# Kernel optimization log

Hardware: AMD Instinct MI355X
Metric: run time of the kernel (lower is better)

The kernel has to match this reference:

```python
import jax, jax.numpy as jnp
import numpy as np
import math

B, N, DEG, C, F0, NCLS = 128, 512, 8, 128, 128, 10
E = B * N * DEG
RATIO = 0.8
K1 = math.ceil(RATIO * N)    # 410
K2 = math.ceil(RATIO * K1)   # 328
K3 = math.ceil(RATIO * K2)   # 263


def setup_inputs() -> dict:
    key = jax.random.key(0)
    ks = jax.random.split(key, 32)
    x = jax.random.normal(ks[0], (B * N, F0), jnp.float32)
    epg = N * DEG
    src_l = jax.random.randint(ks[1], (B, epg), 0, N)
    dst_l = jax.random.randint(ks[2], (B, epg), 0, N)
    off = (jnp.arange(B, dtype=jnp.int32) * N)[:, None]
    edge_src = (src_l + off).reshape(-1).astype(jnp.int32)
    edge_dst = (dst_l + off).reshape(-1).astype(jnp.int32)

    def lin(k, fi, fo):
        return jax.random.normal(k, (fi, fo), jnp.float32) / np.float32(np.sqrt(fi))

    inp = {"x": x, "edge_src": edge_src, "edge_dst": edge_dst}
    i = 3
    for s, fi in (("1", F0), ("2", C), ("3", C)):
        inp["Wroot" + s] = lin(ks[i], fi, C); i += 1
        inp["Wrel" + s] = lin(ks[i], fi, C); i += 1
        inp["brel" + s] = jnp.zeros((C,), jnp.float32)
        inp["p" + s] = jax.random.normal(ks[i], (C,), jnp.float32); i += 1
    inp["W1"] = lin(ks[i], 2 * C, 128); i += 1
    inp["b1"] = jnp.zeros((128,), jnp.float32)
    inp["W2"] = lin(ks[i], 128, 64); i += 1
    inp["b2"] = jnp.zeros((64,), jnp.float32)
    inp["W3"] = lin(ks[i], 64, NCLS); i += 1
    inp["b3"] = jnp.zeros((NCLS,), jnp.float32)
    return inp


def graph_conv(x, src, dst, emask, Wroot, Wrel, brel, num_nodes):
    # PyG GraphConv (aggr='add'): lin_rel(sum_j x_j) + lin_root(x_i)
    msg = x[src] * emask[:, None]                      # masked gather  [E, C]
    agg = jax.ops.segment_sum(msg, dst, num_segments=num_nodes)
    return agg @ Wrel + brel + x @ Wroot


def topk_pool(x, p, src, dst, emask, b, n, k):
    # score = tanh(x . p / ||p||), keep top-k nodes per graph, scale kept x by score
    score = jnp.tanh((x @ p) / jnp.linalg.norm(p))     # [b*n]
    vals, idx = jax.lax.top_k(score.reshape(b, n), k)  # [b, k]
    perm = (idx + (jnp.arange(b, dtype=idx.dtype) * n)[:, None]).reshape(-1)
    x_new = x[perm] * vals.reshape(-1, 1)
    inv = jnp.full((b * n,), -1, jnp.int32).at[perm].set(
        jnp.arange(b * k, dtype=jnp.int32))
    ns, nd = inv[src], inv[dst]
    nmask = emask * (ns >= 0) * (nd >= 0)
    return x_new, jnp.maximum(ns, 0), jnp.maximum(nd, 0), nmask


def readout(h, b, k):
    hb = h.reshape(b, k, -1)
    return jnp.concatenate([hb.max(axis=1), hb.mean(axis=1)], axis=-1)  # gmp||gap


def reference(x, edge_src, edge_dst,
              Wroot1, Wrel1, brel1, p1,
              Wroot2, Wrel2, brel2, p2,
              Wroot3, Wrel3, brel3, p3,
              W1, b1, W2, b2, W3, b3):
    emask = jnp.ones((E,), x.dtype)
    s, d = edge_src, edge_dst

    h = jax.nn.relu(graph_conv(x, s, d, emask, Wroot1, Wrel1, brel1, B * N))
    h, s, d, emask = topk_pool(h, p1, s, d, emask, B, N, K1)
    x1 = readout(h, B, K1)

    h = jax.nn.relu(graph_conv(h, s, d, emask, Wroot2, Wrel2, brel2, B * K1))
    h, s, d, emask = topk_pool(h, p2, s, d, emask, B, K1, K2)
    x2 = readout(h, B, K2)

    h = jax.nn.relu(graph_conv(h, s, d, emask, Wroot3, Wrel3, brel3, B * K2))
    h, s, d, emask = topk_pool(h, p3, s, d, emask, B, K2, K3)
    x3 = readout(h, B, K3)

    g = x1 + x2 + x3                                   # [B, 256]
    g = jax.nn.relu(g @ W1 + b1)                       # dropout is identity in eval
    g = jax.nn.relu(g @ W2 + b2)
    return jax.nn.log_softmax(g @ W3 + b3, axis=-1)    # [B, NCLS]
```

## Files before the change

### kernel.cpp

```cpp
#include <hip/hip_runtime.h>
#include <hip/hip_bf16.h>
#include <math.h>

#define B_G   128
#define N0    512
#define DEG   8
#define CCH   128
#define EPG   (N0*DEG)
#define E_TOTAL (B_G*EPG)
#define K1    410
#define K2    328
#define K3    263
#define NCLS  10

using bf16x8 = __attribute__((ext_vector_type(8))) __bf16;
using f32x4  = __attribute__((ext_vector_type(4))) float;
typedef unsigned short ushort;
typedef unsigned int uint;

__device__ __forceinline__ ushort f2b(float f) {
    uint u = __float_as_uint(f);
    u += 0x7fffu + ((u >> 16) & 1u);
    return (ushort)(u >> 16);
}
__device__ __forceinline__ float b2f(ushort h) {
    return __uint_as_float(((uint)h) << 16);
}
__device__ __forceinline__ void split2(float v, ushort& hi, ushort& lo) {
    hi = f2b(v);
    lo = f2b(v - b2f(hi));
}
__device__ __forceinline__ uint pksplit(float v) {
    ushort h, l; split2(v, h, l);
    return (uint)h | ((uint)l << 16);
}
__device__ __forceinline__ float unpk(uint u) {
    return __uint_as_float(u << 16) + __uint_as_float(u & 0xffff0000u);
}

__global__ __launch_bounds__(512) void setup_kernel(
        const float* __restrict__ x0, uint* __restrict__ xp, int n4,
        const float* __restrict__ Wrel0, const float* __restrict__ Wroot0,
        const float* __restrict__ Wrel1, const float* __restrict__ Wroot1,
        const float* __restrict__ Wrel2, const float* __restrict__ Wroot2,
        ushort* __restrict__ Bph, ushort* __restrict__ Bpl,
        const int* __restrict__ es, const int* __restrict__ ed,
        int* __restrict__ indptr0, int* __restrict__ counts0, ushort* __restrict__ srclist0) {
    __shared__ uint epk[EPG];
    __shared__ int cnt[512], pref[512], curs[512];
    if (blockIdx.x < B_G) {
        int b = blockIdx.x, tid = threadIdx.x;
        cnt[tid] = 0;
        __syncthreads();
        int base = b * EPG;
        for (int i = tid; i < EPG; i += 512) {
            int s = es[base + i] & (N0 - 1);
            int d = ed[base + i] & (N0 - 1);
            epk[i] = (uint)s | ((uint)d << 16);
            atomicAdd(&cnt[d], 1);
        }
        __syncthreads();
        pref[tid] = cnt[tid];
        __syncthreads();
        for (int off = 1; off < 512; off <<= 1) {
            int v = (tid >= off) ? pref[tid - off] : 0;
            __syncthreads();
            pref[tid] += v;
            __syncthreads();
        }
        int excl = tid ? pref[tid - 1] : 0;
        indptr0[b * N0 + tid] = base + excl;
        counts0[b * N0 + tid] = cnt[tid];
        curs[tid] = excl;
        __syncthreads();
        for (int i = tid; i < EPG; i += 512) {
            uint wv = epk[i];
            int dl = wv >> 16;
            int pos = atomicAdd(&curs[dl], 1);
            srclist0[base + pos] = (ushort)(wv & 0xFFFFu);
        }
    } else {
        int i = (blockIdx.x - B_G) * 512 + threadIdx.x;
        if (i < n4) {
            float4 v = ((const float4*)x0)[i];
            uint4 o;
            o.x = pksplit(v.x); o.y = pksplit(v.y); o.z = pksplit(v.z); o.w = pksplit(v.w);
            ((uint4*)xp)[i] = o;
        }
        if (i < 3 * 32768) {
            int layer = i >> 15, rem = i & 32767;
            int j = rem & 7, lane = (rem >> 3) & 63, cf = (rem >> 9) & 7, ks = rem >> 12;
            int k = ks * 32 + (lane >> 4) * 8 + j;
            int c = cf * 16 + (lane & 15);
            const float* Wrel  = layer == 0 ? Wrel0  : layer == 1 ? Wrel1  : Wrel2;
            const float* Wroot = layer == 0 ? Wroot0 : layer == 1 ? Wroot1 : Wroot2;
            float v = (k < 128) ? Wrel[k * 128 + c] : Wroot[(k - 128) * 128 + c];
            ushort hi, lo; split2(v, hi, lo);
            Bph[i] = hi; Bpl[i] = lo;
        }
    }
}

__global__ __launch_bounds__(1024) void aggregate(
        const uint* __restrict__ hin, const int* __restrict__ perm,
        const float* __restrict__ pval,
        const int* __restrict__ indptr, const int* __restrict__ counts,
        const ushort* __restrict__ srclist,
        uint* __restrict__ aggp, int n) {
    extern __shared__ float slab[];
    int b = blockIdx.x >> 2, q = blockIdx.x & 3;
    int tid = threadIdx.x;
    for (int t = tid; t < n * 8; t += 1024) {
        int nd = t >> 3, c4 = t & 7;
        int gid = b * n + nd;
        size_t old = perm ? (size_t)perm[gid] : (size_t)gid;
        float v = perm ? pval[gid] : 1.f;
        uint4 u = *(const uint4*)&hin[old * CCH + q * 32 + c4 * 4];
        *(float4*)&slab[nd * 32 + c4 * 4] =
            make_float4(unpk(u.x) * v, unpk(u.y) * v, unpk(u.z) * v, unpk(u.w) * v);
    }
    __syncthreads();
    int wave = tid >> 6, lane = tid & 63;
    int gl = lane >> 3;
    int sub = lane & 7;
    int ngroups = (n + 7) >> 3;
    for (int g = wave; g < ngroups; g += 16) {
        int d = g * 8 + gl;
        bool act = d < n;
        int beg = 0, cnt = 0;
        if (act) { beg = indptr[b * n + d]; cnt = counts[b * n + d]; }
        float4 acc = make_float4(0.f, 0.f, 0.f, 0.f);
        int id_next = (cnt > 0) ? (int)srclist[beg] : 0;
        for (int j = 0; j < cnt; j++) {
            int id = id_next;
            if (j + 1 < cnt) id_next = (int)srclist[beg + j + 1];
            const float4 v = *(const float4*)&slab[id * 32 + sub * 4];
            acc.x += v.x; acc.y += v.y; acc.z += v.z; acc.w += v.w;
        }
        if (act) {
            uint4 o;
            o.x = pksplit(acc.x); o.y = pksplit(acc.y);
            o.z = pksplit(acc.z); o.w = pksplit(acc.w);
            *(uint4*)&aggp[(size_t)(b * n + d) * CCH + q * 32 + sub * 4] = o;
        }
    }
}

__global__ __launch_bounds__(512, 4) void transform_mfma(
        const uint* __restrict__ aggp, const uint* __restrict__ hin,
        const int* __restrict__ perm, const float* __restrict__ pval,
        const ushort* __restrict__ Bph, const ushort* __restrict__ Bpl,
        const float* __restrict__ brel, const float* __restrict__ pvec,
        uint* __restrict__ hout, float* __restrict__ score) {
    __shared__ ushort ldsBh[16384];
    __shared__ ushort ldsBl[16384];
    int tid = threadIdx.x;
    int wave = tid >> 6, lane = tid & 63;
    int r = lane & 15, kb = lane >> 4;
    int rows0 = blockIdx.x * 128 + wave * 16;
    int gid = rows0 + r;
    size_t oldrow = perm ? (size_t)perm[gid] : (size_t)gid;
    float rv = perm ? pval[gid] : 1.f;

    f32x4 acc[8];
#pragma unroll
    for (int cf = 0; cf < 8; cf++) acc[cf] = (f32x4)(0.f);

    union U16 { uint u[4]; bf16x8 v; };

#pragma unroll
    for (int half = 0; half < 2; half++) {
        if (half) __syncthreads();
#pragma unroll
        for (int i = 0; i < 4; i++) {
            int idx = tid + i * 512;
            ((uint4*)ldsBh)[idx] = ((const uint4*)(Bph + half * 16384))[idx];
            ((uint4*)ldsBl)[idx] = ((const uint4*)(Bpl + half * 16384))[idx];
        }
        __syncthreads();
        const uint* A = half ? hin : aggp;
        size_t abase = half ? oldrow * CCH : (size_t)gid * CCH;
#pragma unroll
        for (int ks4 = 0; ks4 < 4; ks4++) {
            size_t rowbase = abase + ks4 * 32 + kb * 8;
            uint4 ua = *(const uint4*)&A[rowbase];
            uint4 ub = *(const uint4*)&A[rowbase + 4];
            U16 ah, al;
            if (half && perm) {
                float c[8] = {unpk(ua.x) * rv, unpk(ua.y) * rv, unpk(ua.z) * rv,
                              unpk(ua.w) * rv, unpk(ub.x) * rv, unpk(ub.y) * rv,
                              unpk(ub.z) * rv, unpk(ub.w) * rv};
#pragma unroll
                for (int p2 = 0; p2 < 4; p2++) {
                    ushort h0, l0, h1, l1;
                    split2(c[2 * p2], h0, l0);
                    split2(c[2 * p2 + 1], h1, l1);
                    ah.u[p2] = (uint)h0 | ((uint)h1 << 16);
                    al.u[p2] = (uint)l0 | ((uint)l1 << 16);
                }
            } else {
                ah.u[0] = (ua.x & 0xffffu) | (ua.y << 16);
                ah.u[1] = (ua.z & 0xffffu) | (ua.w << 16);
                ah.u[2] = (ub.x & 0xffffu) | (ub.y << 16);
                ah.u[3] = (ub.z & 0xffffu) | (ub.w << 16);
                al.u[0] = (ua.x >> 16) | (ua.y & 0xffff0000u);
                al.u[1] = (ua.z >> 16) | (ua.w & 0xffff0000u);
                al.u[2] = (ub.x >> 16) | (ub.y & 0xffff0000u);
                al.u[3] = (ub.z >> 16) | (ub.w & 0xffff0000u);
            }
#pragma unroll
            for (int cf = 0; cf < 8; cf++) {
                bf16x8 bh = *(const bf16x8*)&ldsBh[((ks4 * 8 + cf) * 64 + lane) * 8];
                bf16x8 bl = *(const bf16x8*)&ldsBl[((ks4 * 8 + cf) * 64 + lane) * 8];
                acc[cf] = __builtin_amdgcn_mfma_f32_16x16x32_bf16(ah.v, bl, acc[cf], 0, 0, 0);
                acc[cf] = __builtin_amdgcn_mfma_f32_16x16x32_bf16(al.v, bh, acc[cf], 0, 0, 0);
                acc[cf] = __builtin_amdgcn_mfma_f32_16x16x32_bf16(ah.v, bh, acc[cf], 0, 0, 0);
            }
        }
    }

    float pv[8], bb[8], q = 0.f;
#pragma unroll
    for (int cf = 0; cf < 8; cf++) {
        pv[cf] = pvec[cf * 16 + r];
        bb[cf] = brel[cf * 16 + r];
        q += pv[cf] * pv[cf];
    }
    float dots[4] = {0.f, 0.f, 0.f, 0.f};
#pragma unroll
    for (int cf = 0; cf < 8; cf++) {
#pragma unroll
        for (int reg = 0; reg < 4; reg++) {
            float v = acc[cf][reg] + bb[cf];
            v = v > 0.f ? v : 0.f;
            hout[(size_t)(rows0 + kb * 4 + reg) * CCH + cf * 16 + r] = pksplit(v);
            dots[reg] += v * pv[cf];
        }
    }
#pragma unroll
    for (int off = 1; off < 16; off <<= 1) {
        q += __shfl_xor(q, off);
#pragma unroll
        for (int reg = 0; reg < 4; reg++) dots[reg] += __shfl_xor(dots[reg], off);
    }
    if (r == 0) {
        float inv_norm = rsqrtf(q);
#pragma unroll
        for (int reg = 0; reg < 4; reg++)
            score[rows0 + kb * 4 + reg] = tanhf(dots[reg] * inv_norm);
    }
}

__global__ __launch_bounds__(512) void pool_kernel(
        const float* __restrict__ score, const uint* __restrict__ hp,
        int* __restrict__ perm_out, float* __restrict__ pval_out,
        float* __restrict__ gpart,
        const int* __restrict__ indptr_in, const int* __restrict__ counts_in,
        const ushort* __restrict__ srclist_in,
        int* __restrict__ indptr_out, int* __restrict__ counts_out,
        ushort* __restrict__ srclist_out,
        int n, int k, int layer, int last) {
    int b = blockIdx.x >> 2, q = blockIdx.x & 3;
    int tid = threadIdx.x;
    __shared__ unsigned long long keys[512];
    __shared__ short invl[512];
    __shared__ float wmax[8][128], wsum[8][128];
    __shared__ int cnt[512], pref[512];
    {
        unsigned long long key = 0ull;
        if (tid < n) {
            uint u = __float_as_uint(score[b * n + tid]);
            u = (u & 0x80000000u) ? ~u : (u | 0x80000000u);
            key = ((unsigned long long)u << 32) | (uint)(~tid);
        }
        keys[tid] = key;
        invl[tid] = -1;
    }
    __syncthreads();
    for (int kk2 = 2; kk2 <= 512; kk2 <<= 1) {
        for (int j = kk2 >> 1; j > 0; j >>= 1) {
            int s = tid, sxj = s ^ j;
            if (sxj > s) {
                unsigned long long a = keys[s], c = keys[sxj];
                bool doSwap = ((s & kk2) == 0) ? (a < c) : (a > c);
                if (doSwap) { keys[s] = c; keys[sxj] = a; }
            }
            __syncthreads();
        }
    }
    if (tid < k) {
        int node = (int)(~(uint)keys[tid]);
        invl[node] = (short)tid;
    }
    __syncthreads();

    if (q == 0) {
        if (last) return;
        int node = -1, beg = 0, c = 0, nk = 0;
        if (tid < k) {
            unsigned long long key = keys[tid];
            node = (int)(~(uint)key);
            uint tu = (uint)(key >> 32);
            uint su = (tu & 0x80000000u) ? (tu & 0x7fffffffu) : ~tu;
            perm_out[b * k + tid] = b * n + node;
            pval_out[b * k + tid] = __uint_as_float(su);
            beg = indptr_in[b * n + node];
            c = counts_in[b * n + node];
            for (int t = 0; t < c; t++)
                if (invl[srclist_in[beg + t]] >= 0) nk++;
        }
        cnt[tid] = (tid < k) ? nk : 0;
        __syncthreads();
        pref[tid] = cnt[tid];
        __syncthreads();
        for (int off = 1; off < 512; off <<= 1) {
            int v = (tid >= off) ? pref[tid - off] : 0;
            __syncthreads();
            pref[tid] += v;
            __syncthreads();
        }
        if (tid < k) {
            int excl = tid ? pref[tid - 1] : 0;
            indptr_out[b * k + tid] = b * EPG + excl;
            counts_out[b * k + tid] = nk;
            int pos = b * EPG + excl;
            for (int t = 0; t < c; t++) {
                int ns = invl[srclist_in[beg + t]];
                if (ns >= 0) srclist_out[pos++] = (ushort)ns;
            }
        }
    } else {
        int p = q - 1;
        int wave = tid >> 6, lane = tid & 63;
        float mx0 = -1e30f, mx1 = -1e30f, sm0 = 0.f, sm1 = 0.f;
        for (int j = p + 3 * wave; j < k; j += 24) {
            unsigned long long key = keys[j];
            int node = (int)(~(uint)key);
            uint tu = (uint)(key >> 32);
            uint su = (tu & 0x80000000u) ? (tu & 0x7fffffffu) : ~tu;
            float v = __uint_as_float(su);
            uint2 u = ((const uint2*)(hp + (size_t)(b * n + node) * CCH))[lane];
            float c0 = unpk(u.x) * v;
            float c1 = unpk(u.y) * v;
            mx0 = fmaxf(mx0, c0); sm0 += c0;
            mx1 = fmaxf(mx1, c1); sm1 += c1;
        }
        wmax[wave][2 * lane] = mx0; wmax[wave][2 * lane + 1] = mx1;
        wsum[wave][2 * lane] = sm0; wsum[wave][2 * lane + 1] = sm1;
        __syncthreads();
        if (tid < 128) {
            float m = wmax[0][tid], s = wsum[0][tid];
#pragma unroll
            for (int w = 1; w < 8; w++) { m = fmaxf(m, wmax[w][tid]); s += wsum[w][tid]; }
            float* gp = gpart + ((size_t)(layer * 3 + p) * B_G + b) * 256;
            gp[tid] = m;
            gp[128 + tid] = s;
        }
    }
}

__global__ __launch_bounds__(128) void mlp_kernel(const float* __restrict__ gpart,
        const float* __restrict__ W1, const float* __restrict__ b1,
        const float* __restrict__ W2, const float* __restrict__ b2,
        const float* __restrict__ W3, const float* __restrict__ b3,
        float* __restrict__ out) {
    int b = blockIdx.x, t = threadIdx.x;
    __shared__ float gs[256], h1[128], h2[64], lg[10];
    const float kdiv[3] = {(float)K1, (float)K2, (float)K3};
    float a0 = 0.f, a1 = 0.f;
#pragma unroll
    for (int l = 0; l < 3; l++) {
        float m = -1e30f, s = 0.f;
#pragma unroll
        for (int p = 0; p < 3; p++) {
            const float* gp = gpart + ((size_t)(l * 3 + p) * B_G + b) * 256;
            m = fmaxf(m, gp[t]);
            s += gp[128 + t];
        }
        a0 += m;
        a1 += s / kdiv[l];
    }
    gs[t] = a0;
    gs[128 + t] = a1;
    __syncthreads();
    {
        float a = b1[t];
        for (int c = 0; c < 256; c++) a += gs[c] * W1[c * 128 + t];
        h1[t] = fmaxf(a, 0.f);
    }
    __syncthreads();
    if (t < 64) {
        float a = b2[t];
        for (int c = 0; c < 128; c++) a += h1[c] * W2[c * 64 + t];
        h2[t] = fmaxf(a, 0.f);
    }
    __syncthreads();
    if (t < 10) {
        float a = b3[t];
        for (int c = 0; c < 64; c++) a += h2[c] * W3[c * 10 + t];
        lg[t] = a;
    }
    __syncthreads();
    if (t < 10) {
        float m = lg[0];
        for (int i = 1; i < 10; i++) m = fmaxf(m, lg[i]);
        float s = 0.f;
        for (int i = 0; i < 10; i++) s += expf(lg[i] - m);
        out[b * 10 + t] = lg[t] - m - logf(s);
    }
}

extern "C" void kernel_launch(void* const* d_in, const int* in_sizes, int n_in,
                              void* d_out, int out_size, void* d_ws, size_t ws_size,
                              hipStream_t stream) {
    (void)in_sizes; (void)n_in; (void)out_size; (void)ws_size;
    const float* x0 = (const float*)d_in[0];
    const int* es = (const int*)d_in[1];
    const int* ed = (const int*)d_in[2];
    const float* Wroot[3] = {(const float*)d_in[3], (const float*)d_in[7], (const float*)d_in[11]};
    const float* Wrel[3]  = {(const float*)d_in[4], (const float*)d_in[8], (const float*)d_in[12]};
    const float* brel[3]  = {(const float*)d_in[5], (const float*)d_in[9], (const float*)d_in[13]};
    const float* pvec[3]  = {(const float*)d_in[6], (const float*)d_in[10], (const float*)d_in[14]};
    const float* W1 = (const float*)d_in[15];
    const float* b1 = (const float*)d_in[16];
    const float* W2 = (const float*)d_in[17];
    const float* b2 = (const float*)d_in[18];
    const float* W3 = (const float*)d_in[19];
    const float* b3 = (const float*)d_in[20];

    size_t off = 0;
    char* base = (char*)d_ws;
    auto alloc = [&](size_t bytes) -> void* {
        void* p = base + off;
        off += (bytes + 255) & ~(size_t)255;
        return p;
    };
    const size_t FEATP = (size_t)(B_G * N0) * CCH * 4;
    uint* P0 = (uint*)alloc(FEATP);
    uint* P1 = (uint*)alloc(FEATP);
    uint* P2 = (uint*)alloc(FEATP);
    ushort* Bph = (ushort*)alloc((size_t)3 * 32768 * 2);
    ushort* Bpl = (ushort*)alloc((size_t)3 * 32768 * 2);
    int* iptA = (int*)alloc((size_t)(B_G * N0) * 4);
    int* cntA = (int*)alloc((size_t)(B_G * N0) * 4);
    ushort* srcA = (ushort*)alloc((size_t)E_TOTAL * 2);
    int* iptB = (int*)alloc((size_t)(B_G * N0) * 4);
    int* cntB = (int*)alloc((size_t)(B_G * N0) * 4);
    ushort* srcB = (ushort*)alloc((size_t)E_TOTAL * 2);
    int* permA = (int*)alloc((size_t)(B_G * K1) * 4);
    float* pvalA = (float*)alloc((size_t)(B_G * K1) * 4);
    int* permB = (int*)alloc((size_t)(B_G * K1) * 4);
    float* pvalB = (float*)alloc((size_t)(B_G * K1) * 4);
    float* score = (float*)alloc((size_t)(B_G * N0) * 4);
    float* gpart = (float*)alloc((size_t)3 * 3 * B_G * 256 * 4);

    const int N4 = B_G * N0 * CCH / 4;
    setup_kernel<<<B_G + (N4 + 511) / 512, 512, 0, stream>>>(
        x0, P2, N4, Wrel[0], Wroot[0], Wrel[1], Wroot[1], Wrel[2], Wroot[2],
        Bph, Bpl, es, ed, iptA, cntA, srcA);

    aggregate<<<4 * B_G, 1024, (size_t)N0 * 32 * 4, stream>>>(
        P2, nullptr, nullptr, iptA, cntA, srcA, P1, N0);
    transform_mfma<<<B_G * N0 / 128, 512, 0, stream>>>(
        P1, P2, nullptr, nullptr, Bph, Bpl, brel[0], pvec[0], P0, score);
    pool_kernel<<<4 * B_G, 512, 0, stream>>>(
        score, P0, permA, pvalA, gpart, iptA, cntA, srcA, iptB, cntB, srcB,
        N0, K1, 0, 0);

    aggregate<<<4 * B_G, 1024, (size_t)K1 * 32 * 4, stream>>>(
        P0, permA, pvalA, iptB, cntB, srcB, P1, K1);
    transform_mfma<<<B_G * K1 / 128, 512, 0, stream>>>(
        P1, P0, permA, pvalA, Bph + 32768, Bpl + 32768, brel[1], pvec[1], P2, score);
    pool_kernel<<<4 * B_G, 512, 0, stream>>>(
        score, P2, permB, pvalB, gpart, iptB, cntB, srcB, iptA, cntA, srcA,
        K1, K2, 1, 0);

    aggregate<<<4 * B_G, 1024, (size_t)K2 * 32 * 4, stream>>>(
        P2, permB, pvalB, iptA, cntA, srcA, P1, K2);
    transform_mfma<<<B_G * K2 / 128, 512, 0, stream>>>(
        P1, P2, permB, pvalB, Bph + 2 * 32768, Bpl + 2 * 32768, brel[2], pvec[2], P0, score);
    pool_kernel<<<4 * B_G, 512, 0, stream>>>(
        score, P0, nullptr, nullptr, gpart, iptA, cntA, srcA, iptB, cntB, srcB,
        K2, K3, 2, 1);

    mlp_kernel<<<B_G, 128, 0, stream>>>(gpart, W1, b1, W2, b2, W3, b3, (float*)d_out);
}
```

Measured before the change: 203.2 us.

## Fuse top-k pooling with next-layer aggregation and drop input bf16 split pass

Pooling now gathers the kept, score-scaled rows into a padded LDS slab. It computes the readout max and mean from that slab, rebuilds the filtered CSR in shared memory, and runs the next layer's neighbour aggregation in the same kernel, so the separate aggregate launches and their global re-gathers go away. The first layer reads fp32 x directly in both aggregation and the root path of the transform, which removes the setup pass that packed x into split bf16. Each of the four channel-quarter blocks now recomputes the CSR filtering redundantly, and the LDS footprint per block grows.

New measurement: 195.5 us. 3.8% less time.

```diff
diff --git a/kernel.cpp b/kernel.cpp
--- a/kernel.cpp
+++ b/kernel.cpp
@@ -37,9 +37,13 @@
 __device__ __forceinline__ float unpk(uint u) {
     return __uint_as_float(u << 16) + __uint_as_float(u & 0xffff0000u);
 }
+__device__ __forceinline__ float keyval(unsigned long long key) {
+    uint tu = (uint)(key >> 32);
+    uint su = (tu & 0x80000000u) ? (tu & 0x7fffffffu) : ~tu;
+    return __uint_as_float(su);
+}
 
 __global__ __launch_bounds__(512) void setup_kernel(
-        const float* __restrict__ x0, uint* __restrict__ xp, int n4,
         const float* __restrict__ Wrel0, const float* __restrict__ Wroot0,
         const float* __restrict__ Wrel1, const float* __restrict__ Wroot1,
         const float* __restrict__ Wrel2, const float* __restrict__ Wroot2,
@@ -81,12 +85,6 @@
         }
     } else {
         int i = (blockIdx.x - B_G) * 512 + threadIdx.x;
-        if (i < n4) {
-            float4 v = ((const float4*)x0)[i];
-            uint4 o;
-            o.x = pksplit(v.x); o.y = pksplit(v.y); o.z = pksplit(v.z); o.w = pksplit(v.w);
-            ((uint4*)xp)[i] = o;
-        }
         if (i < 3 * 32768) {
             int layer = i >> 15, rem = i & 32767;
             int j = rem & 7, lane = (rem >> 3) & 63, cf = (rem >> 9) & 7, ks = rem >> 12;
@@ -101,53 +99,45 @@
     }
 }
 
-__global__ __launch_bounds__(1024) void aggregate(
-        const uint* __restrict__ hin, const int* __restrict__ perm,
-        const float* __restrict__ pval,
+__global__ __launch_bounds__(1024) void aggregate0(
+        const float* __restrict__ xf,
         const int* __restrict__ indptr, const int* __restrict__ counts,
         const ushort* __restrict__ srclist,
-        uint* __restrict__ aggp, int n) {
+        uint* __restrict__ aggp) {
     extern __shared__ float slab[];
     int b = blockIdx.x >> 2, q = blockIdx.x & 3;
     int tid = threadIdx.x;
-    for (int t = tid; t < n * 8; t += 1024) {
+    const float4* xf4 = (const float4*)xf;
+    for (int t = tid; t < N0 * 8; t += 1024) {
         int nd = t >> 3, c4 = t & 7;
-        int gid = b * n + nd;
-        size_t old = perm ? (size_t)perm[gid] : (size_t)gid;
-        float v = perm ? pval[gid] : 1.f;
-        uint4 u = *(const uint4*)&hin[old * CCH + q * 32 + c4 * 4];
-        *(float4*)&slab[nd * 32 + c4 * 4] =
-            make_float4(unpk(u.x) * v, unpk(u.y) * v, unpk(u.z) * v, unpk(u.w) * v);
+        float4 u = xf4[(size_t)(b * N0 + nd) * 32 + q * 8 + c4];
+        *(float4*)&slab[nd * 36 + c4 * 4] = u;
     }
     __syncthreads();
     int wave = tid >> 6, lane = tid & 63;
-    int gl = lane >> 3;
-    int sub = lane & 7;
-    int ngroups = (n + 7) >> 3;
-    for (int g = wave; g < ngroups; g += 16) {
+    int gl = lane >> 3, sub = lane & 7;
+    for (int g = wave; g < N0 / 8; g += 16) {
         int d = g * 8 + gl;
-        bool act = d < n;
-        int beg = 0, cnt = 0;
-        if (act) { beg = indptr[b * n + d]; cnt = counts[b * n + d]; }
+        int beg = indptr[b * N0 + d];
+        int cnt = counts[b * N0 + d];
         float4 acc = make_float4(0.f, 0.f, 0.f, 0.f);
         int id_next = (cnt > 0) ? (int)srclist[beg] : 0;
         for (int j = 0; j < cnt; j++) {
             int id = id_next;
             if (j + 1 < cnt) id_next = (int)srclist[beg + j + 1];
-            const float4 v = *(const float4*)&slab[id * 32 + sub * 4];
+            const float4 v = *(const float4*)&slab[id * 36 + sub * 4];
             acc.x += v.x; acc.y += v.y; acc.z += v.z; acc.w += v.w;
         }
-        if (act) {
-            uint4 o;
-            o.x = pksplit(acc.x); o.y = pksplit(acc.y);
-            o.z = pksplit(acc.z); o.w = pksplit(acc.w);
-            *(uint4*)&aggp[(size_t)(b * n + d) * CCH + q * 32 + sub * 4] = o;
-        }
+        uint4 o;
+        o.x = pksplit(acc.x); o.y = pksplit(acc.y);
+        o.z = pksplit(acc.z); o.w = pksplit(acc.w);
+        *(uint4*)&aggp[(size_t)(b * N0 + d) * CCH + q * 32 + sub * 4] = o;
     }
 }
 
 __global__ __launch_bounds__(512, 4) void transform_mfma(
         const uint* __restrict__ aggp, const uint* __restrict__ hin,
+        const float* __restrict__ rootf,
         const int* __restrict__ perm, const float* __restrict__ pval,
         const ushort* __restrict__ Bph, const ushort* __restrict__ Bpl,
         const float* __restrict__ brel, const float* __restrict__ pvec,
@@ -178,18 +168,14 @@
             ((uint4*)ldsBl)[idx] = ((const uint4*)(Bpl + half * 16384))[idx];
         }
         __syncthreads();
-        const uint* A = half ? hin : aggp;
-        size_t abase = half ? oldrow * CCH : (size_t)gid * CCH;
 #pragma unroll
         for (int ks4 = 0; ks4 < 4; ks4++) {
-            size_t rowbase = abase + ks4 * 32 + kb * 8;
-            uint4 ua = *(const uint4*)&A[rowbase];
-            uint4 ub = *(const uint4*)&A[rowbase + 4];
             U16 ah, al;
-            if (half && perm) {
-                float c[8] = {unpk(ua.x) * rv, unpk(ua.y) * rv, unpk(ua.z) * rv,
-                              unpk(ua.w) * rv, unpk(ub.x) * rv, unpk(ub.y) * rv,
-                              unpk(ub.z) * rv, unpk(ub.w) * rv};
+            if (half && rootf) {
+                const float* R = rootf + (size_t)gid * CCH + ks4 * 32 + kb * 8;
+                float4 f0 = *(const float4*)R;
+                float4 f1 = *(const float4*)(R + 4);
+                float c[8] = {f0.x, f0.y, f0.z, f0.w, f1.x, f1.y, f1.z, f1.w};
 #pragma unroll
                 for (int p2 = 0; p2 < 4; p2++) {
                     ushort h0, l0, h1, l1;
@@ -199,14 +185,33 @@
                     al.u[p2] = (uint)l0 | ((uint)l1 << 16);
                 }
             } else {
-                ah.u[0] = (ua.x & 0xffffu) | (ua.y << 16);
-                ah.u[1] = (ua.z & 0xffffu) | (ua.w << 16);
-                ah.u[2] = (ub.x & 0xffffu) | (ub.y << 16);
-                ah.u[3] = (ub.z & 0xffffu) | (ub.w << 16);
-                al.u[0] = (ua.x >> 16) | (ua.y & 0xffff0000u);
-                al.u[1] = (ua.z >> 16) | (ua.w & 0xffff0000u);
-                al.u[2] = (ub.x >> 16) | (ub.y & 0xffff0000u);
-                al.u[3] = (ub.z >> 16) | (ub.w & 0xffff0000u);
+                const uint* A = half ? hin : aggp;
+                size_t abase = half ? oldrow * CCH : (size_t)gid * CCH;
+                size_t rowbase = abase + ks4 * 32 + kb * 8;
+                uint4 ua = *(const uint4*)&A[rowbase];
+                uint4 ub = *(const uint4*)&A[rowbase + 4];
+                if (half && perm) {
+                    float c[8] = {unpk(ua.x) * rv, unpk(ua.y) * rv, unpk(ua.z) * rv,
+                                  unpk(ua.w) * rv, unpk(ub.x) * rv, unpk(ub.y) * rv,
+                                  unpk(ub.z) * rv, unpk(ub.w) * rv};
+#pragma unroll
+                    for (int p2 = 0; p2 < 4; p2++) {
+                        ushort h0, l0, h1, l1;
+                        split2(c[2 * p2], h0, l0);
+                        split2(c[2 * p2 + 1], h1, l1);
+                        ah.u[p2] = (uint)h0 | ((uint)h1 << 16);
+                        al.u[p2] = (uint)l0 | ((uint)l1 << 16);
+                    }
+                } else {
+                    ah.u[0] = (ua.x & 0xffffu) | (ua.y << 16);
+                    ah.u[1] = (ua.z & 0xffffu) | (ua.w << 16);
+                    ah.u[2] = (ub.x & 0xffffu) | (ub.y << 16);
+                    ah.u[3] = (ub.z & 0xffffu) | (ub.w << 16);
+                    al.u[0] = (ua.x >> 16) | (ua.y & 0xffff0000u);
+                    al.u[1] = (ua.z >> 16) | (ua.w & 0xffff0000u);
+                    al.u[2] = (ub.x >> 16) | (ub.y & 0xffff0000u);
+                    al.u[3] = (ub.z >> 16) | (ub.w & 0xffff0000u);
+                }
             }
 #pragma unroll
             for (int cf = 0; cf < 8; cf++) {
@@ -251,21 +256,23 @@
     }
 }
 
-__global__ __launch_bounds__(512) void pool_kernel(
+__global__ __launch_bounds__(512) void poolagg_kernel(
         const float* __restrict__ score, const uint* __restrict__ hp,
         int* __restrict__ perm_out, float* __restrict__ pval_out,
         float* __restrict__ gpart,
-        const int* __restrict__ indptr_in, const int* __restrict__ counts_in,
-        const ushort* __restrict__ srclist_in,
-        int* __restrict__ indptr_out, int* __restrict__ counts_out,
-        ushort* __restrict__ srclist_out,
-        int n, int k, int layer, int last) {
+        const int* __restrict__ ipt_in, const int* __restrict__ cnt_in,
+        const ushort* __restrict__ src_in,
+        int* __restrict__ ipt_out, int* __restrict__ cnt_out,
+        ushort* __restrict__ src_out,
+        uint* __restrict__ aggout,
+        int n, int k, int do_agg) {
     int b = blockIdx.x >> 2, q = blockIdx.x & 3;
     int tid = threadIdx.x;
     __shared__ unsigned long long keys[512];
     __shared__ short invl[512];
-    __shared__ float wmax[8][128], wsum[8][128];
-    __shared__ int cnt[512], pref[512];
+    __shared__ int cntL[512], prefL[512], iptL[512];
+    __shared__ ushort srcL[EPG];
+    extern __shared__ float slab[];
     {
         unsigned long long key = 0ull;
         if (tid < n) {
@@ -293,68 +300,93 @@
         invl[node] = (short)tid;
     }
     __syncthreads();
-
+    for (int t = tid; t < k * 8; t += 512) {
+        int nd = t >> 3, c4 = t & 7;
+        unsigned long long key = keys[nd];
+        int node = (int)(~(uint)key);
+        float v = keyval(key);
+        uint4 u = *(const uint4*)&hp[(size_t)(b * n + node) * CCH + q * 32 + c4 * 4];
+        *(float4*)&slab[nd * 36 + c4 * 4] =
+            make_float4(unpk(u.x) * v, unpk(u.y) * v, unpk(u.z) * v, unpk(u.w) * v);
+    }
+    __syncthreads();
+    {
+        int ch = tid >> 4, w = tid & 15;
+        float mx = -1e30f, sm = 0.f;
+        for (int r2 = w; r2 < k; r2 += 16) {
+            float v = slab[r2 * 36 + ch];
+            mx = fmaxf(mx, v); sm += v;
+        }
+#pragma unroll
+        for (int off = 1; off < 16; off <<= 1) {
+            mx = fmaxf(mx, __shfl_xor(mx, off));
+            sm += __shfl_xor(sm, off);
+        }
+        if (w == 0) {
+            gpart[b * 256 + q * 32 + ch] = mx;
+            gpart[b * 256 + 128 + q * 32 + ch] = sm / (float)k;
+        }
+    }
+    if (!do_agg) return;
+    int node = -1, beg = 0, c = 0, nk = 0;
+    if (tid < k) {
+        node = (int)(~(uint)keys[tid]);
+        beg = ipt_in[b * n + node];
+        c = cnt_in[b * n + node];
+        for (int t = 0; t < c; t++)
+            if (invl[src_in[beg + t]] >= 0) nk++;
+    }
+    cntL[tid] = (tid < k) ? nk : 0;
+    __syncthreads();
+    prefL[tid] = cntL[tid];
+    __syncthreads();
+    for (int off = 1; off < 512; off <<= 1) {
+        int v = (tid >= off) ? prefL[tid - off] : 0;
+        __syncthreads();
+        prefL[tid] += v;
+        __syncthreads();
+    }
+    int excl = tid ? prefL[tid - 1] : 0;
+    iptL[tid] = excl;
+    if (tid < k) {
+        int pos = excl;
+        for (int t = 0; t < c; t++) {
+            int ns = invl[src_in[beg + t]];
+            if (ns >= 0) srcL[pos++] = (ushort)ns;
+        }
+    }
+    __syncthreads();
     if (q == 0) {
-        if (last) return;
-        int node = -1, beg = 0, c = 0, nk = 0;
+        int tot = prefL[511];
         if (tid < k) {
-            unsigned long long key = keys[tid];
-            node = (int)(~(uint)key);
-            uint tu = (uint)(key >> 32);
-            uint su = (tu & 0x80000000u) ? (tu & 0x7fffffffu) : ~tu;
+            ipt_out[b * k + tid] = b * EPG + excl;
+            cnt_out[b * k + tid] = nk;
             perm_out[b * k + tid] = b * n + node;
-            pval_out[b * k + tid] = __uint_as_float(su);
-            beg = indptr_in[b * n + node];
-            c = counts_in[b * n + node];
-            for (int t = 0; t < c; t++)
-                if (invl[srclist_in[beg + t]] >= 0) nk++;
-        }
-        cnt[tid] = (tid < k) ? nk : 0;
-        __syncthreads();
-        pref[tid] = cnt[tid];
-        __syncthreads();
-        for (int off = 1; off < 512; off <<= 1) {
-            int v = (tid >= off) ? pref[tid - off] : 0;
-            __syncthreads();
-            pref[tid] += v;
-            __syncthreads();
-        }
-        if (tid < k) {
-            int excl = tid ? pref[tid - 1] : 0;
-            indptr_out[b * k + tid] = b * EPG + excl;
-            counts_out[b * k + tid] = nk;
-            int pos = b * EPG + excl;
-            for (int t = 0; t < c; t++) {
-                int ns = invl[srclist_in[beg + t]];
-                if (ns >= 0) srclist_out[pos++] = (ushort)ns;
+            pval_out[b * k + tid] = keyval(keys[tid]);
+        }
+        for (int i = tid; i < tot; i += 512) src_out[b * EPG + i] = srcL[i];
+    }
+    {
+        int wave = tid >> 6, lane = tid & 63;
+        int gl = lane >> 3, sub = lane & 7;
+        int ngroups = (k + 7) >> 3;
+        for (int g = wave; g < ngroups; g += 8) {
+            int d = g * 8 + gl;
+            bool act = d < k;
+            int bg = 0, cc = 0;
+            if (act) { bg = iptL[d]; cc = cntL[d]; }
+            float4 acc = make_float4(0.f, 0.f, 0.f, 0.f);
+            for (int j = 0; j < cc; j++) {
+                int id = (int)srcL[bg + j];
+                const float4 v = *(const float4*)&slab[id * 36 + sub * 4];
+                acc.x += v.x; acc.y += v.y; acc.z += v.z; acc.w += v.w;
             }
-        }
-    } else {
-        int p = q - 1;
-        int wave = tid >> 6, lane = tid & 63;
-        float mx0 = -1e30f, mx1 = -1e30f, sm0 = 0.f, sm1 = 0.f;
-        for (int j = p + 3 * wave; j < k; j += 24) {
-            unsigned long long key = keys[j];
-            int node = (int)(~(uint)key);
-            uint tu = (uint)(key >> 32);
-            uint su = (tu & 0x80000000u) ? (tu & 0x7fffffffu) : ~tu;
-            float v = __uint_as_float(su);
-            uint2 u = ((const uint2*)(hp + (size_t)(b * n + node) * CCH))[lane];
-            float c0 = unpk(u.x) * v;
-            float c1 = unpk(u.y) * v;
-            mx0 = fmaxf(mx0, c0); sm0 += c0;
-            mx1 = fmaxf(mx1, c1); sm1 += c1;
-        }
-        wmax[wave][2 * lane] = mx0; wmax[wave][2 * lane + 1] = mx1;
-        wsum[wave][2 * lane] = sm0; wsum[wave][2 * lane + 1] = sm1;
-        __syncthreads();
-        if (tid < 128) {
-            float m = wmax[0][tid], s = wsum[0][tid];
-#pragma unroll
-            for (int w = 1; w < 8; w++) { m = fmaxf(m, wmax[w][tid]); s += wsum[w][tid]; }
-            float* gp = gpart + ((size_t)(layer * 3 + p) * B_G + b) * 256;
-            gp[tid] = m;
-            gp[128 + tid] = s;
+            if (act) {
+                uint4 o;
+                o.x = pksplit(acc.x); o.y = pksplit(acc.y);
+                o.z = pksplit(acc.z); o.w = pksplit(acc.w);
+                *(uint4*)&aggout[(size_t)(b * k + d) * CCH + q * 32 + sub * 4] = o;
+            }
         }
     }
 }
@@ -366,22 +398,11 @@
         float* __restrict__ out) {
     int b = blockIdx.x, t = threadIdx.x;
     __shared__ float gs[256], h1[128], h2[64], lg[10];
-    const float kdiv[3] = {(float)K1, (float)K2, (float)K3};
-    float a0 = 0.f, a1 = 0.f;
-#pragma unroll
-    for (int l = 0; l < 3; l++) {
-        float m = -1e30f, s = 0.f;
-#pragma unroll
-        for (int p = 0; p < 3; p++) {
-            const float* gp = gpart + ((size_t)(l * 3 + p) * B_G + b) * 256;
-            m = fmaxf(m, gp[t]);
-            s += gp[128 + t];
-        }
-        a0 += m;
-        a1 += s / kdiv[l];
-    }
-    gs[t] = a0;
-    gs[128 + t] = a1;
+    const float* g0 = gpart + ((size_t)0 * B_G + b) * 256;
+    const float* g1 = gpart + ((size_t)1 * B_G + b) * 256;
+    const float* g2 = gpart + ((size_t)2 * B_G + b) * 256;
+    gs[t] = g0[t] + g1[t] + g2[t];
+    gs[128 + t] = g0[128 + t] + g1[128 + t] + g2[128 + t];
     __syncthreads();
     {
         float a = b1[t];
@@ -452,36 +473,33 @@
     int* permB = (int*)alloc((size_t)(B_G * K1) * 4);
     float* pvalB = (float*)alloc((size_t)(B_G * K1) * 4);
     float* score = (float*)alloc((size_t)(B_G * N0) * 4);
-    float* gpart = (float*)alloc((size_t)3 * 3 * B_G * 256 * 4);
-
-    const int N4 = B_G * N0 * CCH / 4;
-    setup_kernel<<<B_G + (N4 + 511) / 512, 512, 0, stream>>>(
-        x0, P2, N4, Wrel[0], Wroot[0], Wrel[1], Wroot[1], Wrel[2], Wroot[2],
+    float* gpart = (float*)alloc((size_t)3 * B_G * 256 * 4);
+
+    setup_kernel<<<B_G + (3 * 32768 + 511) / 512, 512, 0, stream>>>(
+        Wrel[0], Wroot[0], Wrel[1], Wroot[1], Wrel[2], Wroot[2],
         Bph, Bpl, es, ed, iptA, cntA, srcA);
 
-    aggregate<<<4 * B_G, 1024, (size_t)N0 * 32 * 4, stream>>>(
-        P2, nullptr, nullptr, iptA, cntA, srcA, P1, N0);
+    aggregate0<<<4 * B_G, 1024, (size_t)N0 * 36 * 4, stream>>>(
+        x0, iptA, cntA, srcA, P1);
     transform_mfma<<<B_G * N0 / 128, 512, 0, stream>>>(
-        P1, P2, nullptr, nullptr, Bph, Bpl, brel[0], pvec[0], P0, score);
-    pool_kernel<<<4 * B_G, 512, 0, stream>>>(
-        score, P0, permA, pvalA, gpart, iptA, cntA, srcA, iptB, cntB, srcB,
-        N0, K1, 0, 0);
-
-    aggregate<<<4 * B_G, 1024, (size_t)K1 * 32 * 4, stream>>>(
-        P0, permA, pvalA, iptB, cntB, srcB, P1, K1);
+        P1, nullptr, x0, nullptr, nullptr, Bph, Bpl, brel[0], pvec[0], P0, score);
+    poolagg_kernel<<<4 * B_G, 512, (size_t)K1 * 36 * 4, stream>>>(
+        score, P0, permA, pvalA, gpart + (size_t)0 * B_G * 256,
+        iptA, cntA, srcA, iptB, cntB, srcB, P1, N0, K1, 1);
+
     transform_mfma<<<B_G * K1 / 128, 512, 0, stream>>>(
-        P1, P0, permA, pvalA, Bph + 32768, Bpl + 32768, brel[1], pvec[1], P2, score);
-    pool_kernel<<<4 * B_G, 512, 0, stream>>>(
-        score, P2, permB, pvalB, gpart, iptB, cntB, srcB, iptA, cntA, srcA,
-        K1, K2, 1, 0);
-
-    aggregate<<<4 * B_G, 1024, (size_t)K2 * 32 * 4, stream>>>(
-        P2, permB, pvalB, iptA, cntA, srcA, P1, K2);
+        P1, P0, nullptr, permA, pvalA, Bph + 32768, Bpl + 32768,
+        brel[1], pvec[1], P2, score);
+    poolagg_kernel<<<4 * B_G, 512, (size_t)K2 * 36 * 4, stream>>>(
+        score, P2, permB, pvalB, gpart + (size_t)1 * B_G * 256,
+        iptB, cntB, srcB, iptA, cntA, srcA, P1, K1, K2, 1);
+
     transform_mfma<<<B_G * K2 / 128, 512, 0, stream>>>(
-        P1, P2, permB, pvalB, Bph + 2 * 32768, Bpl + 2 * 32768, brel[2], pvec[2], P0, score);
-    pool_kernel<<<4 * B_G, 512, 0, stream>>>(
-        score, P0, nullptr, nullptr, gpart, iptA, cntA, srcA, iptB, cntB, srcB,
-        K2, K3, 2, 1);
+        P1, P2, nullptr, permB, pvalB, Bph + 2 * 32768, Bpl + 2 * 32768,
+        brel[2], pvec[2], P0, score);
+    poolagg_kernel<<<4 * B_G, 512, (size_t)K3 * 36 * 4, stream>>>(
+        score, P0, nullptr, nullptr, gpart + (size_t)2 * B_G * 256,
+        iptA, cntA, srcA, nullptr, nullptr, nullptr, nullptr, K2, K3, 0);
 
     mlp_kernel<<<B_G, 128, 0, stream>>>(gpart, W1, b1, W2, b2, W3, b3, (float*)d_out);
 }
```
